# Kernel optimization log

Measured on AMD Instinct MI355X. Metric: run time of the kernel, lower is better.

Reference implementation:

```python
import jax, jax.numpy as jnp
import numpy as np

N, B, T, IN, H, M, O = 8, 64, 256, 64, 512, 512, 7


def setup_inputs() -> dict:
    key = jax.random.key(0)
    ks = jax.random.split(key, 16)
    s = 1.0 / np.sqrt(H)  # PyTorch LSTM/Linear init scale
    u = lambda k, shape, sc: jax.random.uniform(k, shape, jnp.float32, -sc, sc)
    return {
        "x": jax.random.normal(ks[0], (B, T, IN), jnp.float32),
        # input layer Linear(IN -> H)
        "Win": u(ks[1], (H, IN), 1.0 / np.sqrt(IN)),
        "bin_": u(ks[2], (H,), 1.0 / np.sqrt(IN)),
        # stacked LSTM layer 0 (input H -> hidden H), gates order i,f,g,o
        "W_ih0": u(ks[3], (N, 4 * H, H), s),
        "W_hh0": u(ks[4], (N, 4 * H, H), s),
        "b_ih0": u(ks[5], (N, 4 * H), s),
        "b_hh0": u(ks[6], (N, 4 * H), s),
        # stacked LSTM layer 1
        "W_ih1": u(ks[7], (N, 4 * H, H), s),
        "W_hh1": u(ks[8], (N, 4 * H, H), s),
        "b_ih1": u(ks[9], (N, 4 * H), s),
        "b_hh1": u(ks[10], (N, 4 * H), s),
        # stacked heads: Linear(H->M), LeakyReLU(0.2), Linear(M->O)
        "Wh1": u(ks[11], (N, M, H), s),
        "bh1": u(ks[12], (N, M), s),
        "Wh2": u(ks[13], (N, O, M), 1.0 / np.sqrt(M)),
        "bh2": u(ks[14], (N, O), 1.0 / np.sqrt(M)),
    }


def _lstm_cell(xg, h, c, W_hh, b):
    # xg: precomputable input-gate part [N,B,4H]; h,c: [N,B,H]
    g = xg + jnp.einsum('nbh,ngh->nbg', h, W_hh) + b[:, None, :]
    i, f, gg, o = jnp.split(g, 4, axis=-1)
    c_new = jax.nn.sigmoid(f) * c + jax.nn.sigmoid(i) * jnp.tanh(gg)
    h_new = jax.nn.sigmoid(o) * jnp.tanh(c_new)
    return h_new, c_new


def reference(x, Win, bin_, W_ih0, W_hh0, b_ih0, b_hh0,
              W_ih1, W_hh1, b_ih1, b_hh1, Wh1, bh1, Wh2, bh2):
    # input layer + *10.0
    z = jax.nn.leaky_relu(jnp.einsum('bti,hi->bth', x, Win) + bin_, 0.2) * 10.0  # [B,T,H]

    # precompute input contributions for layer 0 over all timesteps: [T,N,B,4H]
    xg0_all = jnp.einsum('bth,ngh->tnbg', z, W_ih0) + (b_ih0[:, None, :])

    zero = jnp.zeros((N, B, H), z.dtype)

    def step(carry, xg0_t):
        h0, c0, h1, c1 = carry
        h0, c0 = _lstm_cell(xg0_t, h0, c0, W_hh0, b_hh0)
        xg1 = jnp.einsum('nbh,ngh->nbg', h0, W_ih1) + b_ih1[:, None, :]
        h1, c1 = _lstm_cell(xg1, h1, c1, W_hh1, b_hh1)
        return (h0, c0, h1, c1), h1

    _, ys = jax.lax.scan(step, (zero, zero, zero, zero), xg0_all)  # [T,N,B,H]
    y = jnp.transpose(ys, (1, 2, 0, 3))  # [N,B,T,H]

    h = jax.nn.leaky_relu(jnp.einsum('nbth,nmh->nbtm', y, Wh1) + bh1[:, None, None, :], 0.2)
    out = jnp.einsum('nbtm,nom->nbto', h, Wh2) + bh2[:, None, None, :]  # [N,B,T,O]
    return out
```

## Files before the change

kernel.cpp:

```cpp
#include <hip/hip_runtime.h>
#include <hip/hip_bf16.h>

typedef __hip_bfloat16 bf16;
typedef __attribute__((ext_vector_type(8))) short short8;
typedef __attribute__((ext_vector_type(4))) float f32x4;

#define N_ 8
#define B_ 64
#define T_ 256
#define IN_ 64
#define H_ 512
#define G4_ 2048
#define M_ 512
#define O_ 7
#define HP 520

__device__ __forceinline__ float sigf(float x) { return 1.0f / (1.0f + __expf(-x)); }
__device__ __forceinline__ float tanhfast(float x) { return 2.0f / (1.0f + __expf(-2.0f * x)) - 1.0f; }
__device__ __forceinline__ float bfbits2f(unsigned short u) { return __uint_as_float(((unsigned)u) << 16); }

__global__ void cvt_kernel(const float* __restrict__ src, bf16* __restrict__ dst, int n4) {
  for (int i = blockIdx.x * blockDim.x + threadIdx.x; i < n4; i += gridDim.x * blockDim.x) {
    float4 v = ((const float4*)src)[i];
    bf16 t0 = __float2bfloat16(v.x), t1 = __float2bfloat16(v.y);
    bf16 t2 = __float2bfloat16(v.z), t3 = __float2bfloat16(v.w);
    ushort4 o;
    o.x = *(unsigned short*)&t0; o.y = *(unsigned short*)&t1;
    o.z = *(unsigned short*)&t2; o.w = *(unsigned short*)&t3;
    ((ushort4*)dst)[i] = o;
  }
}

__global__ void input_kernel(const float* __restrict__ x, const float* __restrict__ Win,
                             const float* __restrict__ bin, bf16* __restrict__ z) {
  int bid = blockIdx.x;
  int t = bid >> 6;
  int b = bid & 63;
  __shared__ float xr[IN_];
  int tid = threadIdx.x;
  if (tid < IN_) xr[tid] = x[((size_t)b * T_ + t) * IN_ + tid];
  __syncthreads();
  for (int h = tid; h < H_; h += 256) {
    const float* w = Win + (size_t)h * IN_;
    float s = bin[h];
#pragma unroll 16
    for (int i = 0; i < IN_; ++i) s += xr[i] * w[i];
    s = (s > 0.f ? s : 0.2f * s) * 10.f;
    z[((size_t)t * B_ + b) * H_ + h] = __float2bfloat16(s);
  }
}

__device__ __forceinline__ void stage_slab(const bf16* __restrict__ src,
                                           bf16 (*hs)[HP], int tid) {
  unsigned long long va[8], vb[8];
#pragma unroll
  for (int it = 0; it < 8; ++it) {
    int i = tid + it * 512;
    int row = i >> 6, c16 = (i & 63) * 8;
    const unsigned long long* gp = (const unsigned long long*)(src + (size_t)row * H_ + c16);
    va[it] = __hip_atomic_load(gp, __ATOMIC_RELAXED, __HIP_MEMORY_SCOPE_AGENT);
    vb[it] = __hip_atomic_load(gp + 1, __ATOMIC_RELAXED, __HIP_MEMORY_SCOPE_AGENT);
  }
#pragma unroll
  for (int it = 0; it < 8; ++it) {
    int i = tid + it * 512;
    int row = i >> 6, c16 = (i & 63) * 8;
    unsigned long long* lp = (unsigned long long*)&hs[row][c16];
    lp[0] = va[it]; lp[1] = vb[it];
  }
}

__global__ void __launch_bounds__(512, 2) scan_kernel(
    const bf16* __restrict__ z,
    const bf16* __restrict__ Wih0, const bf16* __restrict__ Whh0,
    const float* __restrict__ bih0, const float* __restrict__ bhh0,
    const bf16* __restrict__ Wih1, const bf16* __restrict__ Whh1,
    const float* __restrict__ bih1, const float* __restrict__ bhh1,
    const bf16* __restrict__ Wh1, const float* __restrict__ bh1,
    const float* __restrict__ Wh2, const float* __restrict__ bh2,
    bf16* __restrict__ h0buf, bf16* __restrict__ h1buf,
    bf16* __restrict__ mstage, float* __restrict__ out,
    unsigned* __restrict__ flags)
{
  __shared__ float S0[8][B_][16];
  __shared__ float S1[8][B_][16];
  __shared__ bf16 hs[B_][HP];
  __shared__ bf16 wh1s[16][HP];

  const int tid = threadIdx.x;
  const int lane = tid & 63;
  const int w = tid >> 6;
  const int m = w >> 2;
  const int g = w & 3;
  const int q = lane >> 4;
  const int cl = lane & 15;
  const int bid = blockIdx.x;
  const int n = bid >> 5;
  const int blk = bid & 31;
  const int ub = blk << 4;

  const size_t NBH = (size_t)N_ * B_ * H_;
  const size_t NBM = (size_t)N_ * B_ * M_;

  const size_t wrow = (size_t)n * G4_ * H_ + (size_t)(g * H_ + ub + cl) * H_ + q * 8;
  const bf16* WL0 = (m == 0 ? Wih0 : Whh0) + wrow;
  const bf16* WL1 = (m == 0 ? Wih1 : Whh1) + wrow;
  short8 wl0[16], wl1[16];
#pragma unroll
  for (int kk = 0; kk < 16; ++kk) {
    wl0[kk] = *(const short8*)(WL0 + kk * 32);
    wl1[kk] = *(const short8*)(WL1 + kk * 32);
  }
  const int bi = n * G4_ + g * H_ + ub + cl;
  const float bs0 = (m == 0) ? (bih0[bi] + bhh0[bi]) : 0.f;
  const float bs1 = (m == 0) ? (bih1[bi] + bhh1[bi]) : 0.f;
  const float bh1v = bh1[n * M_ + ub + cl];

  {
    const bf16* wsrc = Wh1 + (size_t)n * M_ * H_ + (size_t)ub * H_;
    for (int i = tid; i < 16 * 64; i += 512) {
      int row = i >> 6, c8 = (i & 63) * 8;
      *(short8*)&wh1s[row][c8] = *(const short8*)(wsrc + (size_t)row * H_ + c8);
    }
  }
  float c0r0 = 0.f, c0r1 = 0.f, c1r0 = 0.f, c1r1 = 0.f;
  __syncthreads();

  unsigned* myflag   = flags + (size_t)n * 64 + blk;
  unsigned* pollbase = flags + (size_t)n * 64;

  for (int s = 0; s < T_ + 3; ++s) {
    const bool doL0 = (s < T_);
    const bool doL1 = (s >= 1 && s <= T_);
    const bool doH1 = (s >= 2 && s <= T_ + 1);
    const bool doH2 = (s >= 3);

    if (s <= T_)
      stage_slab(h0buf + (size_t)((s & 1) ^ 1) * NBH + (size_t)n * B_ * H_, hs, tid);
    __syncthreads();

    if (doL0) {
      if (m == 0) {
        const bf16* A = z + (size_t)s * B_ * H_;
#pragma unroll
        for (int strip = 0; strip < 4; ++strip) {
          f32x4 acc = (f32x4){bs0, bs0, bs0, bs0};
          const bf16* Ap = A + (size_t)(strip * 16 + cl) * H_ + q * 8;
#pragma unroll
          for (int kk = 0; kk < 16; ++kk) {
            short8 a = *(const short8*)(Ap + kk * 32);
            acc = __builtin_amdgcn_mfma_f32_16x16x32_bf16(a, wl0[kk], acc, 0, 0, 0);
          }
#pragma unroll
          for (int r = 0; r < 4; ++r) S0[g][strip * 16 + q * 4 + r][cl] = acc[r];
        }
      } else {
#pragma unroll
        for (int strip = 0; strip < 4; ++strip) {
          f32x4 acc = (f32x4){0.f, 0.f, 0.f, 0.f};
#pragma unroll
          for (int kk = 0; kk < 16; ++kk) {
            short8 a = *(const short8*)&hs[strip * 16 + cl][q * 8 + kk * 32];
            acc = __builtin_amdgcn_mfma_f32_16x16x32_bf16(a, wl0[kk], acc, 0, 0, 0);
          }
#pragma unroll
          for (int r = 0; r < 4; ++r) S0[4 + g][strip * 16 + q * 4 + r][cl] = acc[r];
        }
      }
    }
    if (doL1 && m == 0) {
#pragma unroll
      for (int strip = 0; strip < 4; ++strip) {
        f32x4 acc = (f32x4){bs1, bs1, bs1, bs1};
#pragma unroll
        for (int kk = 0; kk < 16; ++kk) {
          short8 a = *(const short8*)&hs[strip * 16 + cl][q * 8 + kk * 32];
          acc = __builtin_amdgcn_mfma_f32_16x16x32_bf16(a, wl1[kk], acc, 0, 0, 0);
        }
#pragma unroll
        for (int r = 0; r < 4; ++r) S1[g][strip * 16 + q * 4 + r][cl] = acc[r];
      }
    }
    __syncthreads();

    if (s >= 1 && s <= T_ + 1)
      stage_slab(h1buf + (size_t)(s & 1) * NBH + (size_t)n * B_ * H_, hs, tid);
    if (doL0) {
      bf16* h0out = h0buf + (size_t)(s & 1) * NBH + (size_t)n * B_ * H_;
#pragma unroll
      for (int it = 0; it < 2; ++it) {
        int e = tid + it * 512;
        int row = e >> 4, ul = e & 15;
        float gi = S0[0][row][ul] + S0[4][row][ul];
        float gf = S0[1][row][ul] + S0[5][row][ul];
        float gg = S0[2][row][ul] + S0[6][row][ul];
        float go = S0[3][row][ul] + S0[7][row][ul];
        float c = it ? c0r1 : c0r0;
        float cn = sigf(gf) * c + sigf(gi) * tanhfast(gg);
        if (it) c0r1 = cn; else c0r0 = cn;
        float hv = sigf(go) * tanhfast(cn);
        bf16 hb16 = __float2bfloat16(hv);
        unsigned hb = *(unsigned short*)&hb16;
        unsigned nb = (unsigned)__shfl_xor((int)hb, 1, 64);
        if (!(ul & 1)) {
          unsigned word = hb | (nb << 16);
          __hip_atomic_store((unsigned*)(h0out + row * H_ + ub + ul), word,
                             __ATOMIC_RELAXED, __HIP_MEMORY_SCOPE_AGENT);
        }
      }
    }
    __syncthreads();

    if (doL1 && m == 1) {
#pragma unroll
      for (int strip = 0; strip < 4; ++strip) {
        f32x4 acc = (f32x4){0.f, 0.f, 0.f, 0.f};
#pragma unroll
        for (int kk = 0; kk < 16; ++kk) {
          short8 a = *(const short8*)&hs[strip * 16 + cl][q * 8 + kk * 32];
          acc = __builtin_amdgcn_mfma_f32_16x16x32_bf16(a, wl1[kk], acc, 0, 0, 0);
        }
#pragma unroll
        for (int r = 0; r < 4; ++r) S1[4 + g][strip * 16 + q * 4 + r][cl] = acc[r];
      }
    }
    if (doH1 && m == 0) {
      const int tH1 = s - 2;
      f32x4 aH = (f32x4){bh1v, bh1v, bh1v, bh1v};
      for (int kk = 0; kk < H_; kk += 32) {
        short8 a = *(const short8*)&hs[w * 16 + cl][q * 8 + kk];
        short8 b = *(const short8*)&wh1s[cl][q * 8 + kk];
        aH = __builtin_amdgcn_mfma_f32_16x16x32_bf16(a, b, aH, 0, 0, 0);
      }
      bf16* msl = mstage + (size_t)(tH1 & 3) * NBM + (size_t)n * B_ * M_;
#pragma unroll
      for (int r = 0; r < 4; ++r) {
        float v = aH[r];
        v = v > 0.f ? v : 0.2f * v;
        bf16 vb = __float2bfloat16(v);
        unsigned hb = *(unsigned short*)&vb;
        unsigned nb = (unsigned)__shfl_xor((int)hb, 1, 64);
        if (!(cl & 1)) {
          unsigned word = hb | (nb << 16);
          __hip_atomic_store((unsigned*)(msl + (w * 16 + q * 4 + r) * M_ + ub + cl),
                             word, __ATOMIC_RELAXED, __HIP_MEMORY_SCOPE_AGENT);
        }
      }
    }
    __syncthreads();

    if (doL1) {
      const int t = s - 1;
      bf16* h1out = h1buf + (size_t)(t & 1) * NBH + (size_t)n * B_ * H_;
#pragma unroll
      for (int it = 0; it < 2; ++it) {
        int e = tid + it * 512;
        int row = e >> 4, ul = e & 15;
        float gi = S1[0][row][ul] + S1[4][row][ul];
        float gf = S1[1][row][ul] + S1[5][row][ul];
        float gg = S1[2][row][ul] + S1[6][row][ul];
        float go = S1[3][row][ul] + S1[7][row][ul];
        float c = it ? c1r1 : c1r0;
        float cn = sigf(gf) * c + sigf(gi) * tanhfast(gg);
        if (it) c1r1 = cn; else c1r0 = cn;
        float hv = sigf(go) * tanhfast(cn);
        bf16 hb16 = __float2bfloat16(hv);
        unsigned hb = *(unsigned short*)&hb16;
        unsigned nb = (unsigned)__shfl_xor((int)hb, 1, 64);
        if (!(ul & 1)) {
          unsigned word = hb | (nb << 16);
          __hip_atomic_store((unsigned*)(h1out + row * H_ + ub + ul), word,
                             __ATOMIC_RELAXED, __HIP_MEMORY_SCOPE_AGENT);
        }
      }
    }
    __syncthreads();
    if (tid == 0)
      __hip_atomic_store(myflag, (unsigned)(s + 1), __ATOMIC_RELAXED,
                         __HIP_MEMORY_SCOPE_AGENT);

    if (doH2 && (w == 4 || w == 5)) {
      const int tH2 = s - 3;
      const int b = blk * 2 + (w - 4);
      const int o = lane & 7;
      const int oc = o < 7 ? o : 0;
      const int mc = (lane >> 3) * 64;
      const bf16* ms = mstage + (size_t)(tH2 & 3) * NBM + ((size_t)n * B_ + b) * M_ + mc;
      const float* w2p = Wh2 + (size_t)n * O_ * M_ + (size_t)oc * M_ + mc;
      float p = 0.f;
#pragma unroll
      for (int j = 0; j < 64; j += 8) {
        const unsigned long long* mp = (const unsigned long long*)(ms + j);
        unsigned long long u0 = __hip_atomic_load(mp,     __ATOMIC_RELAXED, __HIP_MEMORY_SCOPE_AGENT);
        unsigned long long u1 = __hip_atomic_load(mp + 1, __ATOMIC_RELAXED, __HIP_MEMORY_SCOPE_AGENT);
        float4 w0 = *(const float4*)(w2p + j);
        float4 w1 = *(const float4*)(w2p + j + 4);
        p += bfbits2f((unsigned short)(u0      )) * w0.x
           + bfbits2f((unsigned short)(u0 >> 16)) * w0.y
           + bfbits2f((unsigned short)(u0 >> 32)) * w0.z
           + bfbits2f((unsigned short)(u0 >> 48)) * w0.w
           + bfbits2f((unsigned short)(u1      )) * w1.x
           + bfbits2f((unsigned short)(u1 >> 16)) * w1.y
           + bfbits2f((unsigned short)(u1 >> 32)) * w1.z
           + bfbits2f((unsigned short)(u1 >> 48)) * w1.w;
      }
      p += __shfl_xor(p, 8, 64);
      p += __shfl_xor(p, 16, 64);
      p += __shfl_xor(p, 32, 64);
      if (lane < 7) {
        p += bh2[n * O_ + o];
        out[(((size_t)n * B_ + b) * T_ + tH2) * O_ + o] = p;
      }
    }

    if (w == 7) {
      const unsigned tgt = (unsigned)(s + 1);
      unsigned* fp = pollbase + (lane & 31);
      int spins = 0;
      while (__hip_atomic_load(fp, __ATOMIC_RELAXED, __HIP_MEMORY_SCOPE_AGENT) < tgt) {
        __builtin_amdgcn_s_sleep(2);
        if (++spins >= 256) {
          spins = 0;
          __builtin_amdgcn_fence(__ATOMIC_ACQUIRE, "agent");
        }
      }
    }
    __syncthreads();
  }
}

extern "C" void kernel_launch(void* const* d_in, const int* in_sizes, int n_in,
                              void* d_out, int out_size, void* d_ws, size_t ws_size,
                              hipStream_t stream) {
  (void)in_sizes; (void)n_in; (void)out_size; (void)ws_size;
  const float* x    = (const float*)d_in[0];
  const float* Win  = (const float*)d_in[1];
  const float* bin  = (const float*)d_in[2];
  const float* Wih0 = (const float*)d_in[3];
  const float* Whh0 = (const float*)d_in[4];
  const float* bih0 = (const float*)d_in[5];
  const float* bhh0 = (const float*)d_in[6];
  const float* Wih1 = (const float*)d_in[7];
  const float* Whh1 = (const float*)d_in[8];
  const float* bih1 = (const float*)d_in[9];
  const float* bhh1 = (const float*)d_in[10];
  const float* Wh1  = (const float*)d_in[11];
  const float* bh1  = (const float*)d_in[12];
  const float* Wh2  = (const float*)d_in[13];
  const float* bh2  = (const float*)d_in[14];

  const size_t WLSTM = (size_t)N_ * G4_ * H_;
  const size_t WH1   = (size_t)N_ * M_ * H_;
  const size_t NFLAG = (size_t)N_ * 64;

  char* ws = (char*)d_ws;
  size_t off = 0;
  bf16* z      = (bf16*)(ws + off); off += (size_t)T_ * B_ * H_ * sizeof(bf16);
  bf16* Wih0b  = (bf16*)(ws + off); off += WLSTM * sizeof(bf16);
  bf16* Whh0b  = (bf16*)(ws + off); off += WLSTM * sizeof(bf16);
  bf16* Wih1b  = (bf16*)(ws + off); off += WLSTM * sizeof(bf16);
  bf16* Whh1b  = (bf16*)(ws + off); off += WLSTM * sizeof(bf16);
  bf16* Wh1b   = (bf16*)(ws + off); off += WH1 * sizeof(bf16);
  bf16* h0buf  = (bf16*)(ws + off); off += 2 * (size_t)N_ * B_ * H_ * sizeof(bf16);
  bf16* h1buf  = (bf16*)(ws + off); off += 2 * (size_t)N_ * B_ * H_ * sizeof(bf16);
  bf16* mstage = (bf16*)(ws + off); off += 4 * (size_t)N_ * B_ * M_ * sizeof(bf16);
  unsigned* flags = (unsigned*)(ws + off); off += NFLAG * sizeof(unsigned);

  hipMemsetAsync(h0buf, 0, (char*)(flags + NFLAG) - (char*)h0buf, stream);

  cvt_kernel<<<dim3(2048), dim3(256), 0, stream>>>(Wih0, Wih0b, (int)(WLSTM / 4));
  cvt_kernel<<<dim3(2048), dim3(256), 0, stream>>>(Whh0, Whh0b, (int)(WLSTM / 4));
  cvt_kernel<<<dim3(2048), dim3(256), 0, stream>>>(Wih1, Wih1b, (int)(WLSTM / 4));
  cvt_kernel<<<dim3(2048), dim3(256), 0, stream>>>(Whh1, Whh1b, (int)(WLSTM / 4));
  cvt_kernel<<<dim3(1024), dim3(256), 0, stream>>>(Wh1, Wh1b, (int)(WH1 / 4));

  input_kernel<<<dim3(T_ * B_), dim3(256), 0, stream>>>(x, Win, bin, z);

  scan_kernel<<<dim3(256), dim3(512), 0, stream>>>(
      z, Wih0b, Whh0b, bih0, bhh0, Wih1b, Whh1b, bih1, bhh1,
      Wh1b, bh1, Wh2, bh2, h0buf, h1buf, mstage, (float*)d_out, flags);
}
```

Measured before the change: 4.849 ms.

## Specialize warps per weight matrix and overlap h-state staging with MFMA work

Each of the 8 warps now owns one weight matrix (Whh0, Wih1, Wih0, Whh1) for two gates, instead of every warp holding two matrices for one gate. With that split, some warps can stage the h0/h1 slabs from global memory while others run the input-projection or recurrent MFMAs, so global loads overlap with compute inside a step. Two accumulators per warp add instruction-level parallelism. The cost is more registers for staging (32 u64 values held per thread) and uneven work across warps.

```diff
diff --git a/kernel.cpp b/kernel.cpp
--- a/kernel.cpp
+++ b/kernel.cpp
@@ -17,7 +17,6 @@
 
 __device__ __forceinline__ float sigf(float x) { return 1.0f / (1.0f + __expf(-x)); }
 __device__ __forceinline__ float tanhfast(float x) { return 2.0f / (1.0f + __expf(-2.0f * x)) - 1.0f; }
-__device__ __forceinline__ float bfbits2f(unsigned short u) { return __uint_as_float(((unsigned)u) << 16); }
 
 __global__ void cvt_kernel(const float* __restrict__ src, bf16* __restrict__ dst, int n4) {
   for (int i = blockIdx.x * blockDim.x + threadIdx.x; i < n4; i += gridDim.x * blockDim.x) {
@@ -50,26 +49,6 @@
   }
 }
 
-__device__ __forceinline__ void stage_slab(const bf16* __restrict__ src,
-                                           bf16 (*hs)[HP], int tid) {
-  unsigned long long va[8], vb[8];
-#pragma unroll
-  for (int it = 0; it < 8; ++it) {
-    int i = tid + it * 512;
-    int row = i >> 6, c16 = (i & 63) * 8;
-    const unsigned long long* gp = (const unsigned long long*)(src + (size_t)row * H_ + c16);
-    va[it] = __hip_atomic_load(gp, __ATOMIC_RELAXED, __HIP_MEMORY_SCOPE_AGENT);
-    vb[it] = __hip_atomic_load(gp + 1, __ATOMIC_RELAXED, __HIP_MEMORY_SCOPE_AGENT);
-  }
-#pragma unroll
-  for (int it = 0; it < 8; ++it) {
-    int i = tid + it * 512;
-    int row = i >> 6, c16 = (i & 63) * 8;
-    unsigned long long* lp = (unsigned long long*)&hs[row][c16];
-    lp[0] = va[it]; lp[1] = vb[it];
-  }
-}
-
 __global__ void __launch_bounds__(512, 2) scan_kernel(
     const bf16* __restrict__ z,
     const bf16* __restrict__ Wih0, const bf16* __restrict__ Whh0,
@@ -90,8 +69,8 @@
   const int tid = threadIdx.x;
   const int lane = tid & 63;
   const int w = tid >> 6;
-  const int m = w >> 2;
-  const int g = w & 3;
+  const int p = w & 1;
+  const int gA = 2 * p, gB = 2 * p + 1;
   const int q = lane >> 4;
   const int cl = lane & 15;
   const int bid = blockIdx.x;
@@ -102,18 +81,34 @@
   const size_t NBH = (size_t)N_ * B_ * H_;
   const size_t NBM = (size_t)N_ * B_ * M_;
 
-  const size_t wrow = (size_t)n * G4_ * H_ + (size_t)(g * H_ + ub + cl) * H_ + q * 8;
-  const bf16* WL0 = (m == 0 ? Wih0 : Whh0) + wrow;
-  const bf16* WL1 = (m == 0 ? Wih1 : Whh1) + wrow;
-  short8 wl0[16], wl1[16];
+  const bf16* Wsel;
+  const float *bselA = nullptr, *bselB = nullptr;
+  const float *bsel2A = nullptr, *bsel2B = nullptr;
+  float (*SA)[16];
+  float (*SB)[16];
+  if (w < 2)      { Wsel = Whh0; SA = S0[4 + gA]; SB = S0[4 + gB]; }
+  else if (w < 4) { Wsel = Wih1; SA = S1[gA];     SB = S1[gB];
+                    bselA = bih1; bselB = bhh1; }
+  else if (w < 6) { Wsel = Wih0; SA = S0[gA];     SB = S0[gB];
+                    bselA = bih0; bselB = bhh0; }
+  else            { Wsel = Whh1; SA = S1[4 + gA]; SB = S1[4 + gB]; }
+  (void)bsel2A; (void)bsel2B;
+
+  const size_t wrowA = (size_t)n * G4_ * H_ + (size_t)(gA * H_ + ub + cl) * H_ + q * 8;
+  const size_t wrowB = (size_t)n * G4_ * H_ + (size_t)(gB * H_ + ub + cl) * H_ + q * 8;
+  short8 wlA[16], wlB[16];
 #pragma unroll
   for (int kk = 0; kk < 16; ++kk) {
-    wl0[kk] = *(const short8*)(WL0 + kk * 32);
-    wl1[kk] = *(const short8*)(WL1 + kk * 32);
-  }
-  const int bi = n * G4_ + g * H_ + ub + cl;
-  const float bs0 = (m == 0) ? (bih0[bi] + bhh0[bi]) : 0.f;
-  const float bs1 = (m == 0) ? (bih1[bi] + bhh1[bi]) : 0.f;
+    wlA[kk] = *(const short8*)(Wsel + wrowA + kk * 32);
+    wlB[kk] = *(const short8*)(Wsel + wrowB + kk * 32);
+  }
+  float bA = 0.f, bB = 0.f;
+  if (bselA) {
+    const int iA = n * G4_ + gA * H_ + ub + cl;
+    const int iB = n * G4_ + gB * H_ + ub + cl;
+    bA = bselA[iA] + bselB[iA];
+    bB = bselA[iB] + bselB[iB];
+  }
   const float bh1v = bh1[n * M_ + ub + cl];
 
   {
@@ -134,57 +129,101 @@
     const bool doL1 = (s >= 1 && s <= T_);
     const bool doH1 = (s >= 2 && s <= T_ + 1);
     const bool doH2 = (s >= 3);
-
-    if (s <= T_)
-      stage_slab(h0buf + (size_t)((s & 1) ^ 1) * NBH + (size_t)n * B_ * H_, hs, tid);
-    __syncthreads();
-
-    if (doL0) {
-      if (m == 0) {
-        const bf16* A = z + (size_t)s * B_ * H_;
+    const bool st0  = (s <= T_);
+    const bool st1  = (s >= 1 && s <= T_ + 1);
+
+    if (w < 4) {
+      if (st0) {
+        const bf16* src = h0buf + (size_t)((s & 1) ^ 1) * NBH + (size_t)n * B_ * H_;
+#pragma unroll
+        for (int rd = 0; rd < 2; ++rd) {
+          unsigned long long va[16];
+#pragma unroll
+          for (int it = 0; it < 8; ++it) {
+            int i = tid + (rd * 8 + it) * 256;
+            int row = i >> 6, c16 = i & 63;
+            const unsigned long long* gp =
+                (const unsigned long long*)(src + (size_t)row * H_ + c16 * 8);
+            va[it * 2]     = __hip_atomic_load(gp,     __ATOMIC_RELAXED, __HIP_MEMORY_SCOPE_AGENT);
+            va[it * 2 + 1] = __hip_atomic_load(gp + 1, __ATOMIC_RELAXED, __HIP_MEMORY_SCOPE_AGENT);
+          }
+#pragma unroll
+          for (int it = 0; it < 8; ++it) {
+            int i = tid + (rd * 8 + it) * 256;
+            int row = i >> 6, c16 = i & 63;
+            unsigned long long* lp = (unsigned long long*)&hs[row][c16 * 8];
+            lp[0] = va[it * 2]; lp[1] = va[it * 2 + 1];
+          }
+        }
+      }
+    } else if (w < 6 && doL0) {
+      const bf16* A = z + (size_t)s * B_ * H_;
+#pragma unroll
+      for (int strip = 0; strip < 4; ++strip) {
+        f32x4 aA = (f32x4){bA, bA, bA, bA};
+        f32x4 aB = (f32x4){bB, bB, bB, bB};
+        const bf16* Ap = A + (size_t)(strip * 16 + cl) * H_ + q * 8;
+#pragma unroll
+        for (int kk = 0; kk < 16; ++kk) {
+          short8 a = *(const short8*)(Ap + kk * 32);
+          aA = __builtin_amdgcn_mfma_f32_16x16x32_bf16(a, wlA[kk], aA, 0, 0, 0);
+          aB = __builtin_amdgcn_mfma_f32_16x16x32_bf16(a, wlB[kk], aB, 0, 0, 0);
+        }
+#pragma unroll
+        for (int r = 0; r < 4; ++r) {
+          SA[strip * 16 + q * 4 + r][cl] = aA[r];
+          SB[strip * 16 + q * 4 + r][cl] = aB[r];
+        }
+      }
+    }
+    __syncthreads();
+
+    unsigned long long st[32];
+    if (w < 4) {
+      const bool act = (w < 2) ? doL0 : doL1;
+      if (act) {
 #pragma unroll
         for (int strip = 0; strip < 4; ++strip) {
-          f32x4 acc = (f32x4){bs0, bs0, bs0, bs0};
-          const bf16* Ap = A + (size_t)(strip * 16 + cl) * H_ + q * 8;
-#pragma unroll
-          for (int kk = 0; kk < 16; ++kk) {
-            short8 a = *(const short8*)(Ap + kk * 32);
-            acc = __builtin_amdgcn_mfma_f32_16x16x32_bf16(a, wl0[kk], acc, 0, 0, 0);
-          }
-#pragma unroll
-          for (int r = 0; r < 4; ++r) S0[g][strip * 16 + q * 4 + r][cl] = acc[r];
-        }
-      } else {
-#pragma unroll
-        for (int strip = 0; strip < 4; ++strip) {
-          f32x4 acc = (f32x4){0.f, 0.f, 0.f, 0.f};
+          f32x4 aA = (f32x4){bA, bA, bA, bA};
+          f32x4 aB = (f32x4){bB, bB, bB, bB};
 #pragma unroll
           for (int kk = 0; kk < 16; ++kk) {
             short8 a = *(const short8*)&hs[strip * 16 + cl][q * 8 + kk * 32];
-            acc = __builtin_amdgcn_mfma_f32_16x16x32_bf16(a, wl0[kk], acc, 0, 0, 0);
+            aA = __builtin_amdgcn_mfma_f32_16x16x32_bf16(a, wlA[kk], aA, 0, 0, 0);
+            aB = __builtin_amdgcn_mfma_f32_16x16x32_bf16(a, wlB[kk], aB, 0, 0, 0);
           }
 #pragma unroll
-          for (int r = 0; r < 4; ++r) S0[4 + g][strip * 16 + q * 4 + r][cl] = acc[r];
-        }
-      }
-    }
-    if (doL1 && m == 0) {
-#pragma unroll
-      for (int strip = 0; strip < 4; ++strip) {
-        f32x4 acc = (f32x4){bs1, bs1, bs1, bs1};
-#pragma unroll
-        for (int kk = 0; kk < 16; ++kk) {
-          short8 a = *(const short8*)&hs[strip * 16 + cl][q * 8 + kk * 32];
-          acc = __builtin_amdgcn_mfma_f32_16x16x32_bf16(a, wl1[kk], acc, 0, 0, 0);
-        }
-#pragma unroll
-        for (int r = 0; r < 4; ++r) S1[g][strip * 16 + q * 4 + r][cl] = acc[r];
-      }
-    }
-    __syncthreads();
-
-    if (s >= 1 && s <= T_ + 1)
-      stage_slab(h1buf + (size_t)(s & 1) * NBH + (size_t)n * B_ * H_, hs, tid);
+          for (int r = 0; r < 4; ++r) {
+            SA[strip * 16 + q * 4 + r][cl] = aA[r];
+            SB[strip * 16 + q * 4 + r][cl] = aB[r];
+          }
+        }
+      }
+    } else if (st1) {
+      const bf16* src = h1buf + (size_t)(s & 1) * NBH + (size_t)n * B_ * H_;
+      const int l = tid - 256;
+#pragma unroll
+      for (int it = 0; it < 16; ++it) {
+        int i = l + it * 256;
+        int row = i >> 6, c16 = i & 63;
+        const unsigned long long* gp =
+            (const unsigned long long*)(src + (size_t)row * H_ + c16 * 8);
+        st[it * 2]     = __hip_atomic_load(gp,     __ATOMIC_RELAXED, __HIP_MEMORY_SCOPE_AGENT);
+        st[it * 2 + 1] = __hip_atomic_load(gp + 1, __ATOMIC_RELAXED, __HIP_MEMORY_SCOPE_AGENT);
+      }
+    }
+    __syncthreads();
+
+    if (w >= 4 && st1) {
+      const int l = tid - 256;
+#pragma unroll
+      for (int it = 0; it < 16; ++it) {
+        int i = l + it * 256;
+        int row = i >> 6, c16 = i & 63;
+        unsigned long long* lp = (unsigned long long*)&hs[row][c16 * 8];
+        lp[0] = st[it * 2]; lp[1] = st[it * 2 + 1];
+      }
+    }
     if (doL0) {
       bf16* h0out = h0buf + (size_t)(s & 1) * NBH + (size_t)n * B_ * H_;
 #pragma unroll
@@ -211,20 +250,25 @@
     }
     __syncthreads();
 
-    if (doL1 && m == 1) {
+    if (w >= 6 && doL1) {
 #pragma unroll
       for (int strip = 0; strip < 4; ++strip) {
-        f32x4 acc = (f32x4){0.f, 0.f, 0.f, 0.f};
+        f32x4 aA = (f32x4){0.f, 0.f, 0.f, 0.f};
+        f32x4 aB = (f32x4){0.f, 0.f, 0.f, 0.f};
 #pragma unroll
         for (int kk = 0; kk < 16; ++kk) {
           short8 a = *(const short8*)&hs[strip * 16 + cl][q * 8 + kk * 32];
-          acc = __builtin_amdgcn_mfma_f32_16x16x32_bf16(a, wl1[kk], acc, 0, 0, 0);
-        }
-#pragma unroll
-        for (int r = 0; r < 4; ++r) S1[4 + g][strip * 16 + q * 4 + r][cl] = acc[r];
-      }
-    }
-    if (doH1 && m == 0) {
+          aA = __builtin_amdgcn_mfma_f32_16x16x32_bf16(a, wlA[kk], aA, 0, 0, 0);
+          aB = __builtin_amdgcn_mfma_f32_16x16x32_bf16(a, wlB[kk], aB, 0, 0, 0);
+        }
+#pragma unroll
+        for (int r = 0; r < 4; ++r) {
+          SA[strip * 16 + q * 4 + r][cl] = aA[r];
+          SB[strip * 16 + q * 4 + r][cl] = aB[r];
+        }
+      }
+    }
+    if (w < 4 && doH1) {
       const int tH1 = s - 2;
       f32x4 aH = (f32x4){bh1v, bh1v, bh1v, bh1v};
       for (int kk = 0; kk < H_; kk += 32) {
@@ -287,7 +331,7 @@
       const int mc = (lane >> 3) * 64;
       const bf16* ms = mstage + (size_t)(tH2 & 3) * NBM + ((size_t)n * B_ + b) * M_ + mc;
       const float* w2p = Wh2 + (size_t)n * O_ * M_ + (size_t)oc * M_ + mc;
-      float p = 0.f;
+      float pr = 0.f;
 #pragma unroll
       for (int j = 0; j < 64; j += 8) {
         const unsigned long long* mp = (const unsigned long long*)(ms + j);
@@ -295,21 +339,21 @@
         unsigned long long u1 = __hip_atomic_load(mp + 1, __ATOMIC_RELAXED, __HIP_MEMORY_SCOPE_AGENT);
         float4 w0 = *(const float4*)(w2p + j);
         float4 w1 = *(const float4*)(w2p + j + 4);
-        p += bfbits2f((unsigned short)(u0      )) * w0.x
-           + bfbits2f((unsigned short)(u0 >> 16)) * w0.y
-           + bfbits2f((unsigned short)(u0 >> 32)) * w0.z
-           + bfbits2f((unsigned short)(u0 >> 48)) * w0.w
-           + bfbits2f((unsigned short)(u1      )) * w1.x
-           + bfbits2f((unsigned short)(u1 >> 16)) * w1.y
-           + bfbits2f((unsigned short)(u1 >> 32)) * w1.z
-           + bfbits2f((unsigned short)(u1 >> 48)) * w1.w;
-      }
-      p += __shfl_xor(p, 8, 64);
-      p += __shfl_xor(p, 16, 64);
-      p += __shfl_xor(p, 32, 64);
+        pr += __uint_as_float((unsigned)(u0 & 0xffffu) << 16) * w0.x
+            + __uint_as_float((unsigned)((u0 >> 16) & 0xffffu) << 16) * w0.y
+            + __uint_as_float((unsigned)((u0 >> 32) & 0xffffu) << 16) * w0.z
+            + __uint_as_float((unsigned)((u0 >> 48) & 0xffffu) << 16) * w0.w
+            + __uint_as_float((unsigned)(u1 & 0xffffu) << 16) * w1.x
+            + __uint_as_float((unsigned)((u1 >> 16) & 0xffffu) << 16) * w1.y
+            + __uint_as_float((unsigned)((u1 >> 32) & 0xffffu) << 16) * w1.z
+            + __uint_as_float((unsigned)((u1 >> 48) & 0xffffu) << 16) * w1.w;
+      }
+      pr += __shfl_xor(pr, 8, 64);
+      pr += __shfl_xor(pr, 16, 64);
+      pr += __shfl_xor(pr, 32, 64);
       if (lane < 7) {
-        p += bh2[n * O_ + o];
-        out[(((size_t)n * B_ + b) * T_ + tH2) * O_ + o] = p;
+        pr += bh2[n * O_ + o];
+        out[(((size_t)n * B_ + b) * T_ + tH2) * O_ + o] = pr;
       }
     }
 
@@ -355,7 +399,7 @@
 
   char* ws = (char*)d_ws;
   size_t off = 0;
-  bf16* z      = (bf16*)(ws + off); off += (size_t)T_ * B_ * H_ * sizeof(bf16);
+  bf16* zb     = (bf16*)(ws + off); off += (size_t)T_ * B_ * H_ * sizeof(bf16);
   bf16* Wih0b  = (bf16*)(ws + off); off += WLSTM * sizeof(bf16);
   bf16* Whh0b  = (bf16*)(ws + off); off += WLSTM * sizeof(bf16);
   bf16* Wih1b  = (bf16*)(ws + off); off += WLSTM * sizeof(bf16);
@@ -374,9 +418,9 @@
   cvt_kernel<<<dim3(2048), dim3(256), 0, stream>>>(Whh1, Whh1b, (int)(WLSTM / 4));
   cvt_kernel<<<dim3(1024), dim3(256), 0, stream>>>(Wh1, Wh1b, (int)(WH1 / 4));
 
-  input_kernel<<<dim3(T_ * B_), dim3(256), 0, stream>>>(x, Win, bin, z);
+  input_kernel<<<dim3(T_ * B_), dim3(256), 0, stream>>>(x, Win, bin, zb);
 
   scan_kernel<<<dim3(256), dim3(512), 0, stream>>>(
-      z, Wih0b, Whh0b, bih0, bhh0, Wih1b, Whh1b, bih1, bhh1,
+      zb, Wih0b, Whh0b, bih0, bhh0, Wih1b, Whh1b, bih1, bhh1,
       Wh1b, bh1, Wh2, bh2, h0buf, h1buf, mstage, (float*)d_out, flags);
 }
```

New measurement: 7.206 ms. 1.49x slower.
